# Optimization experiments

Measured on AMD Instinct MI355X. Metric: run time of the kernel, lower is better.

The kernel has to match this reference:

```python
import jax, jax.numpy as jnp
import numpy as np


def _prelu(x, a):
    # torch.nn.PReLU with per-channel parameter a (broadcast over batch)
    return jnp.where(x >= 0, x, a * x)


def setup_inputs() -> dict:
    key = jax.random.key(0)
    ks = jax.random.split(key, 12)
    B = 8192
    dims = [512, 1024, 1024, 512]  # tardim
    E = 8                          # tctrl = modim[-1]
    scale = 0.02                   # keep activations well-scaled across 3 layers
    inp = {
        "x": jax.random.normal(ks[0], (B, dims[0]), dtype=jnp.float32),
        "weights": jax.random.uniform(ks[1], (E,), dtype=jnp.float32),
    }
    for i in range(3):
        din, dout = dims[i], dims[i + 1]
        inp[f"W{i}"] = jax.random.normal(ks[2 + 3 * i], (E, din, dout), dtype=jnp.float32) * scale
        inp[f"b{i}"] = jax.random.normal(ks[3 + 3 * i], (E, dout), dtype=jnp.float32) * scale
        inp[f"a{i}"] = jnp.full((dout,), 0.25, dtype=jnp.float32)  # PReLU init
    return inp


def reference(x, weights, W0, b0, a0, W1, b1, a1, W2, b2, a2):
    # mie.g: per layer, weighted sum over tctrl expert Linears, then PReLU.
    # sum_j (w_j/sum(w)) * (x @ W_j + b_j) == x @ (sum_j wn_j W_j) + sum_j wn_j b_j,
    # so pre-merge expert weights (tiny contraction) and do one GEMM per layer.
    wn = weights / jnp.sum(weights)  # [E]
    for W, b, a in ((W0, b0, a0), (W1, b1, a1), (W2, b2, a2)):
        Wm = jnp.einsum('e,eio->io', wn, W)  # merged weight [in, out]
        bm = jnp.einsum('e,eo->o', wn, b)    # merged bias   [out]
        x = _prelu(x @ Wm + bm, a)           # [B, out]
    return x
```

## Files before the change

kernel.cpp:

```cpp
#include <hip/hip_runtime.h>
#include <stdint.h>

typedef unsigned short u16;
typedef __attribute__((ext_vector_type(8))) short short8;
typedef __attribute__((ext_vector_type(4))) float float4v;

__device__ __forceinline__ u16 f2bf(float f) {
    union { float f; uint32_t u; } v; v.f = f;
    uint32_t r = v.u + 0x7fffu + ((v.u >> 16) & 1u);
    return (u16)(r >> 16);
}

__device__ __forceinline__ void gload16(const u16* g, u16* l) {
    __builtin_amdgcn_global_load_lds(
        (const __attribute__((address_space(1))) void*)g,
        (__attribute__((address_space(3))) void*)l, 16, 0, 0);
}

__global__ __launch_bounds__(256) void prep_fused(
    const float* __restrict__ x, u16* __restrict__ xbf,
    const float* __restrict__ wts,
    const float* __restrict__ W0, const float* __restrict__ W1, const float* __restrict__ W2,
    u16* __restrict__ W0t, u16* __restrict__ W1t, u16* __restrict__ W2t,
    const float* __restrict__ b0, const float* __restrict__ b1, const float* __restrict__ b2,
    float* __restrict__ bm) {
    __shared__ float tile[32][33];
    const int b = blockIdx.x, tid = threadIdx.x;

    if (b < 4096) {
        int i = (b * 256 + tid) * 4;
        float4 v = *(const float4*)(x + i);
        union { u16 s[4]; uint64_t q; } o;
        o.s[0] = f2bf(v.x); o.s[1] = f2bf(v.y); o.s[2] = f2bf(v.z); o.s[3] = f2bf(v.w);
        *(uint64_t*)(xbf + i) = o.q;
        return;
    }

    float wn[8]; float s = 0.f;
    #pragma unroll
    for (int e = 0; e < 8; ++e) { wn[e] = wts[e]; s += wn[e]; }
    const float inv = 1.0f / s;

    if (b < 6144) {
        const float* W; u16* Wt; int K, N, lb;
        if (b < 4608)      { W = W0; Wt = W0t; K = 512;  N = 1024; lb = b - 4096; }
        else if (b < 5632) { W = W1; Wt = W1t; K = 1024; N = 1024; lb = b - 4608; }
        else               { W = W2; Wt = W2t; K = 1024; N = 512;  lb = b - 5632; }
        const int ntiles = N >> 5;
        const int o0 = (lb % ntiles) * 32, i0 = (lb / ntiles) * 32;
        const int tx = tid & 31, ty = tid >> 5;
        #pragma unroll
        for (int s4 = 0; s4 < 4; ++s4) {
            int il = ty + s4 * 8;
            float acc = 0.f;
            #pragma unroll
            for (int e = 0; e < 8; ++e)
                acc += wn[e] * W[(size_t)e * K * N + (size_t)(i0 + il) * N + o0 + tx];
            tile[il][tx] = acc * inv;
        }
        __syncthreads();
        #pragma unroll
        for (int s4 = 0; s4 < 4; ++s4) {
            int ol = ty + s4 * 8;
            Wt[(size_t)(o0 + ol) * K + i0 + tx] = f2bf(tile[tx][ol]);
        }
        return;
    }

    int t = (b - 6144) * 256 + tid;
    if (t >= 2560) return;
    const float* bp; int o, stride;
    if (t < 1024)      { bp = b0; o = t;        stride = 1024; }
    else if (t < 2048) { bp = b1; o = t - 1024; stride = 1024; }
    else               { bp = b2; o = t - 2048; stride = 512;  }
    float acc = 0.f;
    #pragma unroll
    for (int e = 0; e < 8; ++e) acc += wn[e] * bp[e * stride + o];
    bm[t] = acc * inv;
}

template <bool OUT_F32, int NN_LOG2>
__global__ __launch_bounds__(256) void gemm_bias_prelu(
    const u16* __restrict__ A, const u16* __restrict__ Bt,
    const float* __restrict__ bias, const float* __restrict__ alpha,
    void* __restrict__ outp, int M, int N, int K) {
    __shared__ __align__(16) u16 As[128 * 64];
    __shared__ __align__(16) u16 Bs[128 * 64];
    const int tid = threadIdx.x;

    const int xcd   = blockIdx.x & 7;
    const int inner = blockIdx.x >> 3;
    const int bn    = inner & ((1 << NN_LOG2) - 1);
    const int bmv   = xcd * 8 + (inner >> NN_LOG2);

    const int r0 = tid >> 3;
    const int p  = tid & 7;
    const int c  = p ^ (r0 & 7);
    const u16* Ag = A  + (size_t)(bmv * 128 + r0) * K + c * 8;
    const u16* Bg = Bt + (size_t)(bn * 128 + r0) * K + c * 8;
    u16* Al = As + tid * 8;
    u16* Bl = Bs + tid * 8;

    const int lane = tid & 63, w = tid >> 6;
    const int wm = (w >> 1) * 64, wn = (w & 1) * 64;
    const int l16 = lane & 15, quad = lane >> 4;
    const int xr = l16 & 7;
    const short8* As8 = (const short8*)As;
    const short8* Bs8 = (const short8*)Bs;

    float4v acc[4][4] = {};

    const int nk = K >> 6;
    for (int kt = 0; kt < nk; ++kt) {
        #pragma unroll
        for (int it = 0; it < 4; ++it) {
            gload16(Ag + (size_t)(it * 32) * K, Al + it * 2048);
            gload16(Bg + (size_t)(it * 32) * K, Bl + it * 2048);
        }
        __syncthreads();
        #pragma unroll
        for (int kk = 0; kk < 2; ++kk) {
            const int cb = kk * 4;
            short8 af[4], bf[4];
            #pragma unroll
            for (int mi = 0; mi < 4; ++mi)
                af[mi] = As8[(wm + mi * 16 + l16) * 8 + ((cb + quad) ^ xr)];
            #pragma unroll
            for (int ni = 0; ni < 4; ++ni)
                bf[ni] = Bs8[(wn + ni * 16 + l16) * 8 + ((cb + quad) ^ xr)];
            #pragma unroll
            for (int mi = 0; mi < 4; ++mi)
                #pragma unroll
                for (int ni = 0; ni < 4; ++ni)
                    acc[mi][ni] = __builtin_amdgcn_mfma_f32_16x16x32_bf16(
                        af[mi], bf[ni], acc[mi][ni], 0, 0, 0);
        }
        if (kt + 1 < nk) __syncthreads();
        Ag += 64; Bg += 64;
    }

    const int cbase = bn * 128 + wn + l16;
    float bv[4], av[4];
    #pragma unroll
    for (int ni = 0; ni < 4; ++ni) { bv[ni] = bias[cbase + ni * 16]; av[ni] = alpha[cbase + ni * 16]; }
    const int rbase = bmv * 128 + wm + quad * 4;
    #pragma unroll
    for (int mi = 0; mi < 4; ++mi) {
        #pragma unroll
        for (int reg = 0; reg < 4; ++reg) {
            int r = rbase + mi * 16 + reg;
            #pragma unroll
            for (int ni = 0; ni < 4; ++ni) {
                float v = acc[mi][ni][reg] + bv[ni];
                v = v >= 0.f ? v : av[ni] * v;
                size_t idx = (size_t)r * N + cbase + ni * 16;
                if (OUT_F32) ((float*)outp)[idx] = v;
                else         ((u16*)outp)[idx] = f2bf(v);
            }
        }
    }
}

extern "C" void kernel_launch(void* const* d_in, const int* in_sizes, int n_in,
                              void* d_out, int out_size, void* d_ws, size_t ws_size,
                              hipStream_t stream) {
    const float* x   = (const float*)d_in[0];
    const float* wts = (const float*)d_in[1];
    const float* W0  = (const float*)d_in[2];
    const float* b0  = (const float*)d_in[3];
    const float* a0  = (const float*)d_in[4];
    const float* W1  = (const float*)d_in[5];
    const float* b1  = (const float*)d_in[6];
    const float* a1  = (const float*)d_in[7];
    const float* W2  = (const float*)d_in[8];
    const float* b2  = (const float*)d_in[9];
    const float* a2  = (const float*)d_in[10];
    float* out = (float*)d_out;

    char* ws = (char*)d_ws;
    u16*   xbf  = (u16*)ws;  ws += (size_t)8192 * 512 * 2;
    u16*   act1 = (u16*)ws;  ws += (size_t)8192 * 1024 * 2;
    u16*   act2 = (u16*)ws;  ws += (size_t)8192 * 1024 * 2;
    u16*   W0t  = (u16*)ws;  ws += (size_t)1024 * 512 * 2;
    u16*   W1t  = (u16*)ws;  ws += (size_t)1024 * 1024 * 2;
    u16*   W2t  = (u16*)ws;  ws += (size_t)512 * 1024 * 2;
    float* bm   = (float*)ws;

    prep_fused<<<6154, 256, 0, stream>>>(x, xbf, wts, W0, W1, W2, W0t, W1t, W2t,
                                         b0, b1, b2, bm);

    gemm_bias_prelu<false, 3><<<512, 256, 0, stream>>>(xbf,  W0t, bm,        a0, act1, 8192, 1024, 512);
    gemm_bias_prelu<false, 3><<<512, 256, 0, stream>>>(act1, W1t, bm + 1024, a1, act2, 8192, 1024, 1024);
    gemm_bias_prelu<true,  2><<<256, 256, 0, stream>>>(act2, W2t, bm + 2048, a2, out,  8192, 512, 1024);
}
```

Before: 196.8 us.

## Give each wave private double-buffered LDS slices and drop block barriers in GEMM

The GEMM block tile changes from 128x128 shared by four waves to 256x64, where each wave owns a 64x64 output tile. Each wave loads its own A and B K-slices of 32 into a private, double-buffered LDS region, prefetching the next slice while computing the current one. Manual waitcnt calls replace __syncthreads. The aim is to remove block-wide barriers and overlap global-to-LDS loads with MFMA work. In exchange, waves no longer share A or B data in LDS, which raises global and L2 traffic, and correctness now depends on hand-encoded waitcnt values.

```diff
diff --git a/kernel.cpp b/kernel.cpp
--- a/kernel.cpp
+++ b/kernel.cpp
@@ -16,6 +16,10 @@
         (const __attribute__((address_space(1))) void*)g,
         (__attribute__((address_space(3))) void*)l, 16, 0, 0);
 }
+
+#define WAITCNT_LGKM0  do { __builtin_amdgcn_s_waitcnt(0xC07F); asm volatile("" ::: "memory"); } while (0)
+#define WAITCNT_VM8    do { __builtin_amdgcn_s_waitcnt(0x0F78); asm volatile("" ::: "memory"); } while (0)
+#define WAITCNT_VM0    do { __builtin_amdgcn_s_waitcnt(0x0F70); asm volatile("" ::: "memory"); } while (0)
 
 __global__ __launch_bounds__(256) void prep_fused(
     const float* __restrict__ x, u16* __restrict__ xbf,
@@ -80,70 +84,78 @@
 }
 
 template <bool OUT_F32, int NN_LOG2>
-__global__ __launch_bounds__(256) void gemm_bias_prelu(
+__global__ __launch_bounds__(256, 2) void gemm_bias_prelu(
     const u16* __restrict__ A, const u16* __restrict__ Bt,
     const float* __restrict__ bias, const float* __restrict__ alpha,
     void* __restrict__ outp, int M, int N, int K) {
-    __shared__ __align__(16) u16 As[128 * 64];
-    __shared__ __align__(16) u16 Bs[128 * 64];
+    __shared__ __align__(16) u16 smem[4 * 8192];
     const int tid = threadIdx.x;
+    const int lane = tid & 63, w = tid >> 6;
 
     const int xcd   = blockIdx.x & 7;
     const int inner = blockIdx.x >> 3;
     const int bn    = inner & ((1 << NN_LOG2) - 1);
-    const int bmv   = xcd * 8 + (inner >> NN_LOG2);
-
-    const int r0 = tid >> 3;
-    const int p  = tid & 7;
-    const int c  = p ^ (r0 & 7);
-    const u16* Ag = A  + (size_t)(bmv * 128 + r0) * K + c * 8;
-    const u16* Bg = Bt + (size_t)(bn * 128 + r0) * K + c * 8;
-    u16* Al = As + tid * 8;
-    u16* Bl = Bs + tid * 8;
-
-    const int lane = tid & 63, w = tid >> 6;
-    const int wm = (w >> 1) * 64, wn = (w & 1) * 64;
+    const int bmb   = xcd * 4 + (inner >> NN_LOG2);
+    const int m0    = bmb * 256 + w * 64;
+    const int n0    = bn * 64;
+
+    const int rl = lane >> 2;
+    const int cg = (lane & 3) ^ ((lane >> 3) & 3);
+    const u16* Ag = A  + (size_t)(m0 + rl) * K + cg * 8;
+    const u16* Bg = Bt + (size_t)(n0 + rl) * K + cg * 8;
+
+    u16* slice = smem + w * 8192;
     const int l16 = lane & 15, quad = lane >> 4;
-    const int xr = l16 & 7;
-    const short8* As8 = (const short8*)As;
-    const short8* Bs8 = (const short8*)Bs;
+    const int xr2 = (l16 >> 1) & 3;
 
     float4v acc[4][4] = {};
-
-    const int nk = K >> 6;
+    const int nk = K >> 5;
+
+    #pragma unroll
+    for (int j = 0; j < 4; ++j) {
+        gload16(Ag + (size_t)(j * 16) * K, slice + j * 512 + lane * 8);
+        gload16(Bg + (size_t)(j * 16) * K, slice + 2048 + j * 512 + lane * 8);
+    }
+
     for (int kt = 0; kt < nk; ++kt) {
-        #pragma unroll
-        for (int it = 0; it < 4; ++it) {
-            gload16(Ag + (size_t)(it * 32) * K, Al + it * 2048);
-            gload16(Bg + (size_t)(it * 32) * K, Bl + it * 2048);
-        }
-        __syncthreads();
-        #pragma unroll
-        for (int kk = 0; kk < 2; ++kk) {
-            const int cb = kk * 4;
-            short8 af[4], bf[4];
-            #pragma unroll
-            for (int mi = 0; mi < 4; ++mi)
-                af[mi] = As8[(wm + mi * 16 + l16) * 8 + ((cb + quad) ^ xr)];
+        const int cur = (kt & 1) * 4096;
+        if (kt + 1 < nk) {
+            const int nxt = ((kt + 1) & 1) * 4096;
+            const size_t ko = (size_t)(kt + 1) * 32;
+            WAITCNT_LGKM0;
+            #pragma unroll
+            for (int j = 0; j < 4; ++j) {
+                gload16(Ag + (size_t)(j * 16) * K + ko, slice + nxt + j * 512 + lane * 8);
+                gload16(Bg + (size_t)(j * 16) * K + ko, slice + nxt + 2048 + j * 512 + lane * 8);
+            }
+            WAITCNT_VM8;
+        } else {
+            WAITCNT_VM0;
+        }
+
+        const short8* As8 = (const short8*)(slice + cur);
+        const short8* Bs8 = (const short8*)(slice + cur + 2048);
+        short8 af[4], bf[4];
+        const int pos = quad ^ xr2;
+        #pragma unroll
+        for (int mi = 0; mi < 4; ++mi)
+            af[mi] = As8[(mi * 16 + l16) * 4 + pos];
+        #pragma unroll
+        for (int ni = 0; ni < 4; ++ni)
+            bf[ni] = Bs8[(ni * 16 + l16) * 4 + pos];
+        #pragma unroll
+        for (int mi = 0; mi < 4; ++mi)
             #pragma unroll
             for (int ni = 0; ni < 4; ++ni)
-                bf[ni] = Bs8[(wn + ni * 16 + l16) * 8 + ((cb + quad) ^ xr)];
-            #pragma unroll
-            for (int mi = 0; mi < 4; ++mi)
-                #pragma unroll
-                for (int ni = 0; ni < 4; ++ni)
-                    acc[mi][ni] = __builtin_amdgcn_mfma_f32_16x16x32_bf16(
-                        af[mi], bf[ni], acc[mi][ni], 0, 0, 0);
-        }
-        if (kt + 1 < nk) __syncthreads();
-        Ag += 64; Bg += 64;
-    }
-
-    const int cbase = bn * 128 + wn + l16;
+                acc[mi][ni] = __builtin_amdgcn_mfma_f32_16x16x32_bf16(
+                    af[mi], bf[ni], acc[mi][ni], 0, 0, 0);
+    }
+
+    const int cbase = n0 + l16;
     float bv[4], av[4];
     #pragma unroll
     for (int ni = 0; ni < 4; ++ni) { bv[ni] = bias[cbase + ni * 16]; av[ni] = alpha[cbase + ni * 16]; }
-    const int rbase = bmv * 128 + wm + quad * 4;
+    const int rbase = m0 + quad * 4;
     #pragma unroll
     for (int mi = 0; mi < 4; ++mi) {
         #pragma unroll
@@ -189,7 +201,7 @@
     prep_fused<<<6154, 256, 0, stream>>>(x, xbf, wts, W0, W1, W2, W0t, W1t, W2t,
                                          b0, b1, b2, bm);
 
-    gemm_bias_prelu<false, 3><<<512, 256, 0, stream>>>(xbf,  W0t, bm,        a0, act1, 8192, 1024, 512);
-    gemm_bias_prelu<false, 3><<<512, 256, 0, stream>>>(act1, W1t, bm + 1024, a1, act2, 8192, 1024, 1024);
-    gemm_bias_prelu<true,  2><<<256, 256, 0, stream>>>(act2, W2t, bm + 2048, a2, out,  8192, 512, 1024);
-}
+    gemm_bias_prelu<false, 4><<<512, 256, 0, stream>>>(xbf,  W0t, bm,        a0, act1, 8192, 1024, 512);
+    gemm_bias_prelu<false, 4><<<512, 256, 0, stream>>>(act1, W1t, bm + 1024, a1, act2, 8192, 1024, 1024);
+    gemm_bias_prelu<true,  3><<<256, 256, 0, stream>>>(act2, W2t, bm + 2048, a2, out,  8192, 512, 1024);
+}
```

Measured after the change: 199.0 us. No clear change (+1.1%).
